# Performance work log

Measured on AMD Instinct MI355X. Metric: run time of the kernel, lower is better.

The kernel has to match this reference:

```python
import jax, jax.numpy as jnp
import numpy as np

N, E = 100000, 1600000
IN_C, HID_C, OUT_C = 128, 32, 16


def setup_inputs() -> dict:
    key = jax.random.key(0)
    k1, k2, k3, k4, k5, k6 = jax.random.split(key, 6)
    x = jax.random.normal(k1, (N, IN_C), dtype=jnp.float32)
    edge_index = jax.random.randint(k2, (2, E), 0, N, dtype=jnp.int64)
    # glorot-style init for GCN weights
    W1 = jax.random.normal(k3, (IN_C, HID_C), dtype=jnp.float32) * (1.0 / np.sqrt(IN_C))
    b1 = jnp.zeros((HID_C,), dtype=jnp.float32)
    W2 = jax.random.normal(k4, (HID_C, OUT_C), dtype=jnp.float32) * (1.0 / np.sqrt(HID_C))
    b2 = jnp.zeros((OUT_C,), dtype=jnp.float32)
    return {"x": x, "edge_index": edge_index, "W1": W1, "b1": b1, "W2": W2, "b2": b2}


def _gcn_conv(x, W, b, src, dst, norm, n_nodes):
    # linear transform first (PyG GCNConv order), then normalized scatter-add
    h = x @ W                                  # [N, C_out]
    msg = h[src] * norm[:, None]               # gather + per-edge scale
    agg = jax.ops.segment_sum(msg, dst, num_segments=n_nodes)  # scatter-add
    return agg + b


def reference(x, edge_index, W1, b1, W2, b2):
    n_nodes = x.shape[0]
    loop = jnp.arange(n_nodes, dtype=edge_index.dtype)
    # add self-loops (PyG default add_self_loops=True)
    src = jnp.concatenate([edge_index[0], loop])
    dst = jnp.concatenate([edge_index[1], loop])
    # symmetric normalization: deg computed on graph WITH self-loops
    deg = jax.ops.segment_sum(jnp.ones_like(dst, dtype=x.dtype), dst, num_segments=n_nodes)
    dinv = jnp.where(deg > 0, jax.lax.rsqrt(deg), 0.0)
    norm = dinv[src] * dinv[dst]               # [E + N]

    h = _gcn_conv(x, W1, b1, src, dst, norm, n_nodes)
    h = jax.nn.relu(h)
    out = _gcn_conv(h, W2, b2, src, dst, norm, n_nodes)
    return out
```

## Files before the change

kernel.cpp:

```cpp
#include <hip/hip_runtime.h>
#include <stdint.h>


#define TPB 256

__global__ void k_zero2(unsigned int* __restrict__ a, unsigned int* __restrict__ b, int n) {
    int i = blockIdx.x * blockDim.x + threadIdx.x;
    if (i < n) { a[i] = 0u; b[i] = 0u; }
}

__global__ void k_count(const int* __restrict__ dst, unsigned int* __restrict__ cnt, int E) {
    int stride = gridDim.x * blockDim.x;
    for (int i = blockIdx.x * blockDim.x + threadIdx.x; i < E; i += stride)
        atomicAdd(&cnt[(unsigned int)dst[i]], 1u);
}

__global__ void k_dinv(const unsigned int* __restrict__ cnt, float* __restrict__ dinv, int n) {
    int i = blockIdx.x * blockDim.x + threadIdx.x;
    if (i < n) dinv[i] = rsqrtf(1.0f + (float)cnt[i]);
}

__global__ void k_blocksums(const unsigned int* __restrict__ cnt, unsigned int* __restrict__ partial, int n) {
    __shared__ unsigned int sm[TPB];
    int i = blockIdx.x * TPB + threadIdx.x;
    sm[threadIdx.x] = (i < n) ? cnt[i] : 0u;
    __syncthreads();
    for (int off = TPB / 2; off > 0; off >>= 1) {
        if (threadIdx.x < off) sm[threadIdx.x] += sm[threadIdx.x + off];
        __syncthreads();
    }
    if (threadIdx.x == 0) partial[blockIdx.x] = sm[0];
}

__global__ void k_scanpartials(unsigned int* __restrict__ partial, int nb) {
    __shared__ unsigned int sm[512];
    int t = threadIdx.x;
    unsigned int v = (t < nb) ? partial[t] : 0u;
    sm[t] = v;
    __syncthreads();
    for (int off = 1; off < 512; off <<= 1) {
        unsigned int add = (t >= off) ? sm[t - off] : 0u;
        __syncthreads();
        sm[t] += add;
        __syncthreads();
    }
    if (t < nb) partial[t] = sm[t] - v;
}

__global__ void k_rowptr(const unsigned int* __restrict__ cnt, const unsigned int* __restrict__ partial,
                         unsigned int* __restrict__ rowptr, int n, int E) {
    __shared__ unsigned int sm[TPB];
    int t = threadIdx.x;
    int i = blockIdx.x * TPB + t;
    unsigned int v = (i < n) ? cnt[i] : 0u;
    sm[t] = v;
    __syncthreads();
    for (int off = 1; off < TPB; off <<= 1) {
        unsigned int add = (t >= off) ? sm[t - off] : 0u;
        __syncthreads();
        sm[t] += add;
        __syncthreads();
    }
    if (i < n) rowptr[i] = partial[blockIdx.x] + sm[t] - v;
    if (i == n - 1) rowptr[n] = (unsigned int)E;
}

__global__ void k_fill(const int* __restrict__ ei, const float* __restrict__ dinv,
                       const unsigned int* __restrict__ rowptr, unsigned int* __restrict__ cursor,
                       int2* __restrict__ adj, int E) {
    const int* srcp = ei;
    const int* dstp = ei + E;
    int stride = gridDim.x * blockDim.x;
    for (int i = blockIdx.x * blockDim.x + threadIdx.x; i < E; i += stride) {
        int s = srcp[i], d = dstp[i];
        unsigned int pos = rowptr[d] + atomicAdd(&cursor[d], 1u);
        adj[pos] = make_int2(s, __float_as_int(dinv[s] * dinv[d]));
    }
}

__global__ __launch_bounds__(TPB) void k_gemm1(const float* __restrict__ x, const float* __restrict__ W1,
                                               float* __restrict__ h1, int n) {
    __shared__ float4 smx4[64 * 32];
    __shared__ float4 smw4[32 * 33];
    float* smw = (float*)smw4;
    int t = threadIdx.x;
    int row0 = blockIdx.x * 64;

#pragma unroll
    for (int it = 0; it < 16; ++it) {
        int idx = it * TPB + t;
        int k = idx >> 5, j = idx & 31;
        smw[j * 132 + k] = W1[idx];
    }
    const float4* x4 = (const float4*)x;
    int lim = n * 32;
#pragma unroll
    for (int it = 0; it < 8; ++it) {
        int fo = it * TPB + t;
        int gi = row0 * 32 + fo;
        smx4[fo] = (gi < lim) ? x4[gi] : make_float4(0.f, 0.f, 0.f, 0.f);
    }
    __syncthreads();

    int j = t & 31, rb = (t >> 5) * 8;
    float acc[8] = {0.f, 0.f, 0.f, 0.f, 0.f, 0.f, 0.f, 0.f};
#pragma unroll 4
    for (int k4 = 0; k4 < 32; ++k4) {
        float4 wv = smw4[j * 33 + k4];
#pragma unroll
        for (int i = 0; i < 8; ++i) {
            float4 xv = smx4[(rb + i) * 32 + k4];
            acc[i] = fmaf(xv.x, wv.x, acc[i]);
            acc[i] = fmaf(xv.y, wv.y, acc[i]);
            acc[i] = fmaf(xv.z, wv.z, acc[i]);
            acc[i] = fmaf(xv.w, wv.w, acc[i]);
        }
    }
#pragma unroll
    for (int i = 0; i < 8; ++i) {
        int row = row0 + rb + i;
        if (row < n) h1[(size_t)row * 32 + j] = acc[i];
    }
}

__global__ void k_agg1(const float* __restrict__ h1, const float* __restrict__ dinv,
                       const unsigned int* __restrict__ rowptr, const int2* __restrict__ adj,
                       float* __restrict__ agg1, int n) {
    int t = blockIdx.x * blockDim.x + threadIdx.x;
    if (t >= n * 8) return;
    int node = t >> 3, c4 = (t & 7) * 4;
    float di = dinv[node];
    float di2 = di * di;
    float4 acc = *(const float4*)(h1 + (size_t)node * 32 + c4);
    acc.x *= di2; acc.y *= di2; acc.z *= di2; acc.w *= di2;
    unsigned int e1 = rowptr[node + 1];
    for (unsigned int e = rowptr[node]; e < e1; ++e) {
        int2 a = adj[e];
        float nrm = __int_as_float(a.y);
        float4 hv = *(const float4*)(h1 + (size_t)a.x * 32 + c4);
        acc.x = fmaf(hv.x, nrm, acc.x);
        acc.y = fmaf(hv.y, nrm, acc.y);
        acc.z = fmaf(hv.z, nrm, acc.z);
        acc.w = fmaf(hv.w, nrm, acc.w);
    }
    *(float4*)(agg1 + (size_t)node * 32 + c4) = acc;
}

__global__ __launch_bounds__(TPB) void k_gemm2(const float* __restrict__ agg1, const float* __restrict__ b1,
                                               const float* __restrict__ W2, float* __restrict__ h2, int n) {
    __shared__ float4 sma4[128 * 8];
    __shared__ float4 smw24[16 * 9];
    float* smw2 = (float*)smw24;
    int t = threadIdx.x;
    int row0 = blockIdx.x * 128;

#pragma unroll
    for (int it = 0; it < 2; ++it) {
        int idx = it * TPB + t;
        int k = idx >> 4, j = idx & 15;
        smw2[j * 36 + k] = W2[idx];
    }
    const float4* a4 = (const float4*)agg1;
    const float4* b14 = (const float4*)b1;
    int lim = n * 8;
#pragma unroll
    for (int it = 0; it < 4; ++it) {
        int fo = it * TPB + t;
        int gi = row0 * 8 + fo;
        float4 v = (gi < lim) ? a4[gi] : make_float4(0.f, 0.f, 0.f, 0.f);
        float4 b = b14[fo & 7];
        v.x = fmaxf(v.x + b.x, 0.f);
        v.y = fmaxf(v.y + b.y, 0.f);
        v.z = fmaxf(v.z + b.z, 0.f);
        v.w = fmaxf(v.w + b.w, 0.f);
        sma4[fo] = v;
    }
    __syncthreads();

    int j = t & 15, rb = (t >> 4) * 8;
    float acc[8] = {0.f, 0.f, 0.f, 0.f, 0.f, 0.f, 0.f, 0.f};
#pragma unroll
    for (int k4 = 0; k4 < 8; ++k4) {
        float4 wv = smw24[j * 9 + k4];
#pragma unroll
        for (int i = 0; i < 8; ++i) {
            float4 xv = sma4[(rb + i) * 8 + k4];
            acc[i] = fmaf(xv.x, wv.x, acc[i]);
            acc[i] = fmaf(xv.y, wv.y, acc[i]);
            acc[i] = fmaf(xv.z, wv.z, acc[i]);
            acc[i] = fmaf(xv.w, wv.w, acc[i]);
        }
    }
#pragma unroll
    for (int i = 0; i < 8; ++i) {
        int row = row0 + rb + i;
        if (row < n) h2[(size_t)row * 16 + j] = acc[i];
    }
}

__global__ void k_agg2(const float* __restrict__ h2, const float* __restrict__ dinv,
                       const float* __restrict__ b2,
                       const unsigned int* __restrict__ rowptr, const int2* __restrict__ adj,
                       float* __restrict__ out, int n) {
    int t = blockIdx.x * blockDim.x + threadIdx.x;
    if (t >= n * 4) return;
    int node = t >> 2, c4 = (t & 3) * 4;
    float di = dinv[node];
    float di2 = di * di;
    float4 hv0 = *(const float4*)(h2 + (size_t)node * 16 + c4);
    float4 bv = *(const float4*)(b2 + c4);
    float4 acc = make_float4(fmaf(hv0.x, di2, bv.x), fmaf(hv0.y, di2, bv.y),
                             fmaf(hv0.z, di2, bv.z), fmaf(hv0.w, di2, bv.w));
    unsigned int e1 = rowptr[node + 1];
    for (unsigned int e = rowptr[node]; e < e1; ++e) {
        int2 a = adj[e];
        float nrm = __int_as_float(a.y);
        float4 hv = *(const float4*)(h2 + (size_t)a.x * 16 + c4);
        acc.x = fmaf(hv.x, nrm, acc.x);
        acc.y = fmaf(hv.y, nrm, acc.y);
        acc.z = fmaf(hv.z, nrm, acc.z);
        acc.w = fmaf(hv.w, nrm, acc.w);
    }
    *(float4*)(out + (size_t)node * 16 + c4) = acc;
}

static inline char* align256(char* p) {
    return (char*)(((uintptr_t)p + 255) & ~(uintptr_t)255);
}

extern "C" void kernel_launch(void* const* d_in, const int* in_sizes, int n_in,
                              void* d_out, int out_size, void* d_ws, size_t ws_size,
                              hipStream_t stream) {
    const float* x  = (const float*)d_in[0];
    const int*   ei = (const int*)d_in[1];
    const float* W1 = (const float*)d_in[2];
    const float* b1 = (const float*)d_in[3];
    const float* W2 = (const float*)d_in[4];
    const float* b2 = (const float*)d_in[5];
    float*       out = (float*)d_out;

    int N = in_sizes[0] / 128;
    int E = in_sizes[1] / 2;

    char* p = (char*)d_ws;
    unsigned int* rowptr  = (unsigned int*)p;  p = align256(p + (size_t)(N + 1) * 4);
    unsigned int* cnt     = (unsigned int*)p;  p = align256(p + (size_t)N * 4);
    unsigned int* cursor  = (unsigned int*)p;  p = align256(p + (size_t)N * 4);
    unsigned int* partial = (unsigned int*)p;  p = align256(p + 512 * 4);
    float*        dinv    = (float*)p;         p = align256(p + (size_t)N * 4);
    int2*         adj     = (int2*)p;          p = align256(p + (size_t)E * 8);
    float*        h1      = (float*)p;         p = align256(p + (size_t)N * 32 * 4);
    float*        agg1    = (float*)p;
    float*        h2      = h1;

    int gN = (N + TPB - 1) / TPB;
    int NB = gN;

    k_zero2        <<<gN,   TPB, 0, stream>>>(cnt, cursor, N);
    k_count        <<<2048, TPB, 0, stream>>>(ei + E, cnt, E);
    k_dinv         <<<gN,   TPB, 0, stream>>>(cnt, dinv, N);
    k_blocksums    <<<NB,   TPB, 0, stream>>>(cnt, partial, N);
    k_scanpartials <<<1,    512, 0, stream>>>(partial, NB);
    k_rowptr       <<<NB,   TPB, 0, stream>>>(cnt, partial, rowptr, N, E);
    k_fill         <<<2048, TPB, 0, stream>>>(ei, dinv, rowptr, cursor, adj, E);

    k_gemm1 <<<(N + 63) / 64,          TPB, 0, stream>>>(x, W1, h1, N);
    k_agg1  <<<(N * 8 + TPB - 1) / TPB, TPB, 0, stream>>>(h1, dinv, rowptr, adj, agg1, N);
    k_gemm2 <<<(N + 127) / 128,        TPB, 0, stream>>>(agg1, b1, W2, h2, N);
    k_agg2  <<<(N * 4 + TPB - 1) / TPB, TPB, 0, stream>>>(h2, dinv, b2, rowptr, adj, out, N);
}
```

Before: 358.5 us.

## Partition adjacency fill by destination range per XCD group with vectorized dst reads

Splits the fill kernel's blocks into 8 groups, chosen by block index modulo 8, and each group handles only edges whose destination falls in its node range. The aim is to keep cursor atomics and adjacency writes for a node range local to one XCD's L2, cutting cross-die coherence traffic. Destination indices are read as int4. The trade-off is that every group scans the full destination array, multiplying read traffic by eight.

```diff
diff --git a/kernel.cpp b/kernel.cpp
--- a/kernel.cpp
+++ b/kernel.cpp
@@ -67,12 +67,32 @@
 
 __global__ void k_fill(const int* __restrict__ ei, const float* __restrict__ dinv,
                        const unsigned int* __restrict__ rowptr, unsigned int* __restrict__ cursor,
-                       int2* __restrict__ adj, int E) {
+                       int2* __restrict__ adj, int E, int range) {
     const int* srcp = ei;
     const int* dstp = ei + E;
-    int stride = gridDim.x * blockDim.x;
-    for (int i = blockIdx.x * blockDim.x + threadIdx.x; i < E; i += stride) {
-        int s = srcp[i], d = dstp[i];
+    int g  = blockIdx.x & 7;
+    int lo = g * range;
+    int hi = lo + range;
+    int stride = (gridDim.x >> 3) * blockDim.x;
+    int i0 = (blockIdx.x >> 3) * blockDim.x + threadIdx.x;
+    int nq = E >> 2;
+    const int4* dst4 = (const int4*)dstp;
+    for (int q = i0; q < nq; q += stride) {
+        int4 dv = dst4[q];
+        int base = q * 4;
+#pragma unroll
+        for (int u = 0; u < 4; ++u) {
+            int d = (u == 0) ? dv.x : (u == 1) ? dv.y : (u == 2) ? dv.z : dv.w;
+            if (d < lo || d >= hi) continue;
+            int s = srcp[base + u];
+            unsigned int pos = rowptr[d] + atomicAdd(&cursor[d], 1u);
+            adj[pos] = make_int2(s, __float_as_int(dinv[s] * dinv[d]));
+        }
+    }
+    for (int i = (nq << 2) + i0; i < E; i += stride) {
+        int d = dstp[i];
+        if (d < lo || d >= hi) continue;
+        int s = srcp[i];
         unsigned int pos = rowptr[d] + atomicAdd(&cursor[d], 1u);
         adj[pos] = make_int2(s, __float_as_int(dinv[s] * dinv[d]));
     }
@@ -255,6 +275,7 @@
 
     int gN = (N + TPB - 1) / TPB;
     int NB = gN;
+    int range = (N + 7) / 8;
 
     k_zero2        <<<gN,   TPB, 0, stream>>>(cnt, cursor, N);
     k_count        <<<2048, TPB, 0, stream>>>(ei + E, cnt, E);
@@ -262,7 +283,7 @@
     k_blocksums    <<<NB,   TPB, 0, stream>>>(cnt, partial, N);
     k_scanpartials <<<1,    512, 0, stream>>>(partial, NB);
     k_rowptr       <<<NB,   TPB, 0, stream>>>(cnt, partial, rowptr, N, E);
-    k_fill         <<<2048, TPB, 0, stream>>>(ei, dinv, rowptr, cursor, adj, E);
+    k_fill         <<<2048, TPB, 0, stream>>>(ei, dinv, rowptr, cursor, adj, E, range);
 
     k_gemm1 <<<(N + 63) / 64,          TPB, 0, stream>>>(x, W1, h1, N);
     k_agg1  <<<(N * 8 + TPB - 1) / TPB, TPB, 0, stream>>>(h1, dinv, rowptr, adj, agg1, N);
```

After: 359.0 us. About the same (+0.2%).
